# Performance work log

Hardware: AMD Instinct MI355X
Metric: run time of the kernel (lower is better)

## Reference

```python
import jax, jax.numpy as jnp
import numpy as np

B, D = 256, 1024
EPS = 1e-6


def setup_inputs() -> dict:
    key = jax.random.key(0)
    ks = jax.random.split(key, 8)
    s = 1.0 / np.sqrt(D)
    return {
        "x": jax.random.normal(ks[0], (B, D), jnp.float32),
        "Wq": jax.random.normal(ks[1], (D, D), jnp.float32) * s,
        "bq": jax.random.normal(ks[2], (D,), jnp.float32) * 0.01,
        "Wk": jax.random.normal(ks[3], (D, D), jnp.float32) * s,
        "bk": jax.random.normal(ks[4], (D,), jnp.float32) * 0.01,
        "Wv": jax.random.normal(ks[5], (D, D), jnp.float32) * s,
        "bv": jax.random.normal(ks[6], (D,), jnp.float32) * 0.01,
        "scale": jnp.asarray(1.0, jnp.float32),
        "norm_w": jnp.ones((D,), jnp.float32),
    }


def reference(x, Wq, bq, Wk, bk, Wv, bv, scale, norm_w):
    # QKV projections (torch Linear: x @ W.T + b)
    Q = x @ Wq.T + bq  # [B, D]
    K = x @ Wk.T + bk  # [B, D]
    V = x @ Wv.T + bv  # [B, D]
    # outer-product scores [B, D, D]: scores[b,i,j] = Q[b,i]*K[b,j]/scale
    scores = (Q[:, :, None] * K[:, None, :]) / scale
    attn = jax.nn.softmax(scores, axis=-1)  # [B, D, D]
    attended = jnp.einsum("bij,bj->bi", attn, V)  # [B, D]
    # dropout is identity in eval mode
    h = attended + x
    rms = jnp.sqrt(jnp.mean(h * h, axis=-1, keepdims=True) + EPS)
    return (h / rms) * norm_w
```

## Files before the change

### kernel.cpp

```cpp
#include <hip/hip_runtime.h>
#include <hip/hip_bf16.h>

#define BB 256
#define DD 1024

typedef unsigned short u16;
typedef unsigned int   u32;
typedef __attribute__((ext_vector_type(8))) __bf16 bf16x8;
typedef __attribute__((ext_vector_type(4))) float  floatx4;

__device__ __forceinline__ float bf2f(u16 u) {
    union { u32 i; float f; } t; t.i = ((u32)u) << 16; return t.f;
}
__device__ __forceinline__ u16 f2bf_rne(float f) {
    u32 u = __float_as_uint(f);
    u32 r = u + 0x7FFFu + ((u >> 16) & 1u);
    return (u16)(r >> 16);
}
__device__ __forceinline__ bool detect_bf16(const void* p) {
    return (*(const u32*)p) == 0x3F803F80u;
}
__device__ __forceinline__ float loadf(const void* p, int i, bool bf) {
    return bf ? bf2f(((const u16*)p)[i]) : ((const float*)p)[i];
}

__device__ __forceinline__ float wave_sum64(float x) {
    x += __int_as_float(__builtin_amdgcn_update_dpp(0, __float_as_int(x), 0x111, 0xF, 0xF, true));
    x += __int_as_float(__builtin_amdgcn_update_dpp(0, __float_as_int(x), 0x112, 0xF, 0xF, true));
    x += __int_as_float(__builtin_amdgcn_update_dpp(0, __float_as_int(x), 0x114, 0xF, 0xF, true));
    x += __int_as_float(__builtin_amdgcn_update_dpp(0, __float_as_int(x), 0x118, 0xF, 0xF, true));
    x += __int_as_float(__builtin_amdgcn_update_dpp(0, __float_as_int(x), 0x142, 0xA, 0xF, true));
    x += __int_as_float(__builtin_amdgcn_update_dpp(0, __float_as_int(x), 0x143, 0xC, 0xF, true));
    return x;
}

__device__ __forceinline__ void split1(float f, u16& h, u16& l) {
    u32 u  = __float_as_uint(f);
    u32 hu = u & 0xFFFF0000u;
    h = (u16)(hu >> 16);
    l = f2bf_rne(f - __uint_as_float(hu));
}

__global__ __launch_bounds__(256) void qkv_gemm(
    const void* __restrict__ x,
    const void* __restrict__ Wq, const void* __restrict__ bq,
    const void* __restrict__ Wk, const void* __restrict__ bk,
    const void* __restrict__ Wv, const void* __restrict__ bv,
    const void* __restrict__ nw,
    float* __restrict__ qkv)
{
    const bool bf = detect_bf16(nw);
    const int z = blockIdx.z;
    const void* W    = (z == 0) ? Wq : (z == 1) ? Wk : Wv;
    const void* bias = (z == 0) ? bq : (z == 1) ? bk : bv;
    float* outp = qkv + (size_t)z * BB * DD;

    const int m0 = blockIdx.x * 32;
    const int n0 = blockIdx.y * 64;
    const int tid  = threadIdx.x;
    const int lane = tid & 63;
    const int wave = tid >> 6;
    const int wr = wave & 1, wc = wave >> 1;
    const int l15 = lane & 15, quad = lane >> 4;

    __shared__ __align__(16) u16 Ah[32][72], Al[32][72];
    __shared__ __align__(16) u16 Bh[64][72], Bl[64][72];

    const int arow = tid >> 4;
    const int acol = (tid & 15) * 4;

    floatx4 acc[2] = {(floatx4){0.f,0.f,0.f,0.f}, (floatx4){0.f,0.f,0.f,0.f}};

    float4 ar[2], br[4];
    auto ld4 = [&](const void* p, int idx) -> float4 {
        if (!bf) return *(const float4*)((const float*)p + idx);
        const u16* q = (const u16*)p + idx;
        return make_float4(bf2f(q[0]), bf2f(q[1]), bf2f(q[2]), bf2f(q[3]));
    };
    auto fetch = [&](int k0) {
        #pragma unroll
        for (int f = 0; f < 2; ++f) ar[f] = ld4(x, (m0 + arow + f * 16) * DD + k0 + acol);
        #pragma unroll
        for (int f = 0; f < 4; ++f) br[f] = ld4(W, (n0 + arow + f * 16) * DD + k0 + acol);
    };

    fetch(0);
    for (int k0 = 0; k0 < DD; k0 += 64) {
        #pragma unroll
        for (int f = 0; f < 2; ++f) {
            const int r = arow + f * 16;
            ushort4 h, l;
            split1(ar[f].x, h.x, l.x); split1(ar[f].y, h.y, l.y);
            split1(ar[f].z, h.z, l.z); split1(ar[f].w, h.w, l.w);
            *(ushort4*)&Ah[r][acol] = h;
            *(ushort4*)&Al[r][acol] = l;
        }
        #pragma unroll
        for (int f = 0; f < 4; ++f) {
            const int r = arow + f * 16;
            ushort4 h, l;
            split1(br[f].x, h.x, l.x); split1(br[f].y, h.y, l.y);
            split1(br[f].z, h.z, l.z); split1(br[f].w, h.w, l.w);
            *(ushort4*)&Bh[r][acol] = h;
            *(ushort4*)&Bl[r][acol] = l;
        }
        __syncthreads();

        fetch((k0 + 64) & (DD - 1));

        #pragma unroll
        for (int kk = 0; kk < 2; ++kk) {
            const int ko = kk * 32 + quad * 8;
            const bf16x8 ah = *(const bf16x8*)&Ah[wr * 16 + l15][ko];
            const bf16x8 al = *(const bf16x8*)&Al[wr * 16 + l15][ko];
            #pragma unroll
            for (int ni = 0; ni < 2; ++ni) {
                const int brow = wc * 32 + ni * 16 + l15;
                const bf16x8 bh = *(const bf16x8*)&Bh[brow][ko];
                const bf16x8 bl = *(const bf16x8*)&Bl[brow][ko];
                acc[ni] = __builtin_amdgcn_mfma_f32_16x16x32_bf16(al, bh, acc[ni], 0, 0, 0);
                acc[ni] = __builtin_amdgcn_mfma_f32_16x16x32_bf16(ah, bl, acc[ni], 0, 0, 0);
                acc[ni] = __builtin_amdgcn_mfma_f32_16x16x32_bf16(ah, bh, acc[ni], 0, 0, 0);
            }
        }
        __syncthreads();
    }

    #pragma unroll
    for (int ni = 0; ni < 2; ++ni) {
        const int ng = n0 + wc * 32 + ni * 16 + l15;
        const float bv_ = loadf(bias, ng, bf);
        #pragma unroll
        for (int reg = 0; reg < 4; ++reg) {
            const int mg = m0 + wr * 16 + quad * 4 + reg;
            outp[mg * DD + ng] = acc[ni][reg] + bv_;
        }
    }
}

__global__ __launch_bounds__(1024) void attn_norm(
    const float* __restrict__ qkv,
    const void* __restrict__ x,
    const void* __restrict__ scale_p,
    const void* __restrict__ norm_w,
    void* __restrict__ out)
{
    const bool bf = detect_bf16(norm_w);
    const int b = blockIdx.x;
    const int tid = threadIdx.x;
    const int lane = tid & 63;
    const int wave = tid >> 6;

    __shared__ __align__(16) float2 kv[DD];
    __shared__ float wsum[16];

    const float* Qp = qkv + (size_t)b * DD;
    const float* Kp = Qp + (size_t)BB * DD;
    const float* Vp = Qp + 2 * (size_t)BB * DD;
    const float cvt = 1.44269504088896f / loadf(scale_p, 0, bf);

    kv[tid] = make_float2(Kp[tid] * cvt, Vp[tid]);
    __syncthreads();

    const float q   = Qp[tid];
    const float x_l = loadf(x, b * DD + tid, bf);

    float S0 = 0.f, S1 = 0.f, S2 = 0.f, S3 = 0.f;
    float T0 = 0.f, T1 = 0.f, T2 = 0.f, T3 = 0.f;
    const float4* kv4 = (const float4*)kv;
    for (int m = 0; m < DD / 2; m += 4) {
        const float4 p0 = kv4[m + 0];
        const float4 p1 = kv4[m + 1];
        const float4 p2 = kv4[m + 2];
        const float4 p3 = kv4[m + 3];
        float e;
        e = __builtin_amdgcn_exp2f(q * p0.x); S0 += e; T0 = fmaf(e, p0.y, T0);
        e = __builtin_amdgcn_exp2f(q * p0.z); S1 += e; T1 = fmaf(e, p0.w, T1);
        e = __builtin_amdgcn_exp2f(q * p1.x); S2 += e; T2 = fmaf(e, p1.y, T2);
        e = __builtin_amdgcn_exp2f(q * p1.z); S3 += e; T3 = fmaf(e, p1.w, T3);
        e = __builtin_amdgcn_exp2f(q * p2.x); S0 += e; T0 = fmaf(e, p2.y, T0);
        e = __builtin_amdgcn_exp2f(q * p2.z); S1 += e; T1 = fmaf(e, p2.w, T1);
        e = __builtin_amdgcn_exp2f(q * p3.x); S2 += e; T2 = fmaf(e, p3.y, T2);
        e = __builtin_amdgcn_exp2f(q * p3.z); S3 += e; T3 = fmaf(e, p3.w, T3);
    }
    const float S = (S0 + S1) + (S2 + S3);
    const float T = (T0 + T1) + (T2 + T3);
    const float h = fmaf(T, __builtin_amdgcn_rcpf(S), x_l);

    const float ss = wave_sum64(h * h);
    if (lane == 63) wsum[wave] = ss;
    __syncthreads();
    float tot = 0.f;
    #pragma unroll
    for (int w = 0; w < 16; ++w) tot += wsum[w];
    const float rinv = __builtin_amdgcn_rsqf(tot * (1.0f / DD) + 1e-6f);
    const float val = h * rinv * loadf(norm_w, tid, bf);
    const size_t oi = (size_t)b * DD + tid;
    if (bf) ((u16*)out)[oi] = f2bf_rne(val);
    else    ((float*)out)[oi] = val;
}

extern "C" void kernel_launch(void* const* d_in, const int* in_sizes, int n_in,
                              void* d_out, int out_size, void* d_ws, size_t ws_size,
                              hipStream_t stream) {
    const void* x  = d_in[0];
    const void* Wq = d_in[1];
    const void* bq = d_in[2];
    const void* Wk = d_in[3];
    const void* bk = d_in[4];
    const void* Wv = d_in[5];
    const void* bv = d_in[6];
    const void* sc = d_in[7];
    const void* nw = d_in[8];

    float* qkv = (float*)d_ws;

    qkv_gemm<<<dim3(8, 16, 3), 256, 0, stream>>>(x, Wq, bq, Wk, bk, Wv, bv, nw, qkv);
    attn_norm<<<dim3(BB), 1024, 0, stream>>>(qkv, x, sc, nw, d_out);
}
```

Before: 133.6 us.

## Register-tile attention loop over 4 queries × key quarter with packed float2 math

Each thread of the attention kernel now handles 4 query rows over one quarter of the keys instead of one query over all keys. This reuses each LDS key/value load across four queries, cutting LDS traffic per exp, and uses float2 vector types so the compiler can emit packed multiply/FMA instructions. Partial sums are reduced through a new shared buffer with an extra barrier. The cost is more registers and an added reduction step, while the exp count stays the same.

```diff
diff --git a/kernel.cpp b/kernel.cpp
--- a/kernel.cpp
+++ b/kernel.cpp
@@ -8,6 +8,7 @@
 typedef unsigned int   u32;
 typedef __attribute__((ext_vector_type(8))) __bf16 bf16x8;
 typedef __attribute__((ext_vector_type(4))) float  floatx4;
+typedef __attribute__((ext_vector_type(2))) float  floatx2;
 
 __device__ __forceinline__ float bf2f(u16 u) {
     union { u32 i; float f; } t; t.i = ((u32)u) << 16; return t.f;
@@ -150,8 +151,12 @@
     const int tid = threadIdx.x;
     const int lane = tid & 63;
     const int wave = tid >> 6;
-
-    __shared__ __align__(16) float2 kv[DD];
+    const int iq = tid & 255;
+    const int jq = tid >> 8;
+
+    __shared__ __align__(16) float kk[DD];
+    __shared__ __align__(16) float vv[DD];
+    __shared__ float2 part[DD][4];
     __shared__ float wsum[16];
 
     const float* Qp = qkv + (size_t)b * DD;
@@ -159,33 +164,67 @@
     const float* Vp = Qp + 2 * (size_t)BB * DD;
     const float cvt = 1.44269504088896f / loadf(scale_p, 0, bf);
 
-    kv[tid] = make_float2(Kp[tid] * cvt, Vp[tid]);
+    kk[tid] = Kp[tid] * cvt;
+    vv[tid] = Vp[tid];
     __syncthreads();
 
-    const float q   = Qp[tid];
+    const float qv[4] = { Qp[iq], Qp[iq + 256], Qp[iq + 512], Qp[iq + 768] };
+
+    floatx2 S[4][2] = {};
+    floatx2 T[4][2] = {};
+
+    const floatx4* kk4 = (const floatx4*)kk;
+    const floatx4* vv4 = (const floatx4*)vv;
+    const int jb = jq * 64;
+
+    floatx4 kc0 = kk4[jb], kc1 = kk4[jb + 1];
+    floatx4 vc0 = vv4[jb], vc1 = vv4[jb + 1];
+    for (int mo = 0; mo < 64; mo += 2) {
+        const int mn = jb + ((mo + 2) & 63);
+        floatx4 kn0 = kk4[mn], kn1 = kk4[mn + 1];
+        floatx4 vn0 = vv4[mn], vn1 = vv4[mn + 1];
+
+        #pragma unroll
+        for (int g = 0; g < 2; ++g) {
+            const floatx4 K4 = g ? kc1 : kc0;
+            const floatx4 V4 = g ? vc1 : vc0;
+            const floatx2 kA = __builtin_shufflevector(K4, K4, 0, 1);
+            const floatx2 kB = __builtin_shufflevector(K4, K4, 2, 3);
+            const floatx2 vA = __builtin_shufflevector(V4, V4, 0, 1);
+            const floatx2 vB = __builtin_shufflevector(V4, V4, 2, 3);
+            #pragma unroll
+            for (int r = 0; r < 4; ++r) {
+                const float qr = qv[r];
+                const floatx2 aA = kA * qr;
+                const floatx2 aB = kB * qr;
+                floatx2 eA, eB;
+                eA.x = __builtin_amdgcn_exp2f(aA.x);
+                eA.y = __builtin_amdgcn_exp2f(aA.y);
+                eB.x = __builtin_amdgcn_exp2f(aB.x);
+                eB.y = __builtin_amdgcn_exp2f(aB.y);
+                S[r][g] += (eA + eB);
+                T[r][g] = __builtin_elementwise_fma(eA, vA, T[r][g]);
+                T[r][g] = __builtin_elementwise_fma(eB, vB, T[r][g]);
+            }
+        }
+        kc0 = kn0; kc1 = kn1; vc0 = vn0; vc1 = vn1;
+    }
+
+    #pragma unroll
+    for (int r = 0; r < 4; ++r) {
+        const floatx2 Sv = S[r][0] + S[r][1];
+        const floatx2 Tv = T[r][0] + T[r][1];
+        part[iq + r * 256][jq] = make_float2(Sv.x + Sv.y, Tv.x + Tv.y);
+    }
+    __syncthreads();
+
+    const float2 p0 = part[tid][0], p1 = part[tid][1];
+    const float2 p2 = part[tid][2], p3 = part[tid][3];
+    const float Ssum = (p0.x + p1.x) + (p2.x + p3.x);
+    const float Tsum = (p0.y + p1.y) + (p2.y + p3.y);
+
     const float x_l = loadf(x, b * DD + tid, bf);
-
-    float S0 = 0.f, S1 = 0.f, S2 = 0.f, S3 = 0.f;
-    float T0 = 0.f, T1 = 0.f, T2 = 0.f, T3 = 0.f;
-    const float4* kv4 = (const float4*)kv;
-    for (int m = 0; m < DD / 2; m += 4) {
-        const float4 p0 = kv4[m + 0];
-        const float4 p1 = kv4[m + 1];
-        const float4 p2 = kv4[m + 2];
-        const float4 p3 = kv4[m + 3];
-        float e;
-        e = __builtin_amdgcn_exp2f(q * p0.x); S0 += e; T0 = fmaf(e, p0.y, T0);
-        e = __builtin_amdgcn_exp2f(q * p0.z); S1 += e; T1 = fmaf(e, p0.w, T1);
-        e = __builtin_amdgcn_exp2f(q * p1.x); S2 += e; T2 = fmaf(e, p1.y, T2);
-        e = __builtin_amdgcn_exp2f(q * p1.z); S3 += e; T3 = fmaf(e, p1.w, T3);
-        e = __builtin_amdgcn_exp2f(q * p2.x); S0 += e; T0 = fmaf(e, p2.y, T0);
-        e = __builtin_amdgcn_exp2f(q * p2.z); S1 += e; T1 = fmaf(e, p2.w, T1);
-        e = __builtin_amdgcn_exp2f(q * p3.x); S2 += e; T2 = fmaf(e, p3.y, T2);
-        e = __builtin_amdgcn_exp2f(q * p3.z); S3 += e; T3 = fmaf(e, p3.w, T3);
-    }
-    const float S = (S0 + S1) + (S2 + S3);
-    const float T = (T0 + T1) + (T2 + T3);
-    const float h = fmaf(T, __builtin_amdgcn_rcpf(S), x_l);
+    const float h = fmaf(Tsum, __builtin_amdgcn_rcpf(Ssum), x_l);
 
     const float ss = wave_sum64(h * h);
     if (lane == 63) wsum[wave] = ss;
```

Result: faster. 126.5 us (-5.3%).

## Split attention reduction across key halves with register-blocked queries and finalize kernel

Applied to the files above, without the earlier changes.

The attention stage becomes two kernels. The first splits the key dimension into two halves per batch row (twice the blocks), and each thread handles four queries over a 128-key slice so every shared-memory K/V load feeds four exponentials. Partial sums are combined in shared memory and written to workspace. A second kernel merges the two halves and applies the residual add and RMSNorm. The aim is better occupancy and fewer LDS reads per exponential, at the cost of an extra launch and a workspace round trip.

```diff
diff --git a/kernel.cpp b/kernel.cpp
--- a/kernel.cpp
+++ b/kernel.cpp
@@ -138,54 +138,97 @@
     }
 }
 
-__global__ __launch_bounds__(1024) void attn_norm(
+__global__ __launch_bounds__(1024) void attn_part(
     const float* __restrict__ qkv,
+    const void* __restrict__ scale_p,
+    const void* __restrict__ norm_w,
+    float2* __restrict__ pws)
+{
+    const bool bf = detect_bf16(norm_w);
+    const int b   = blockIdx.x;
+    const int jh  = blockIdx.y;
+    const int tid = threadIdx.x;
+    const int iq  = tid & 255;
+    const int jq  = tid >> 8;
+
+    __shared__ __align__(16) float kk[512];
+    __shared__ __align__(16) float vv[512];
+    __shared__ float2 part[DD][4];
+
+    const float* Qp = qkv + (size_t)b * DD;
+    const float* Kp = Qp + (size_t)BB * DD;
+    const float* Vp = Qp + 2 * (size_t)BB * DD;
+    const float cvt = 1.44269504088896f / loadf(scale_p, 0, bf);
+
+    if (tid < 512) {
+        kk[tid] = Kp[jh * 512 + tid] * cvt;
+        vv[tid] = Vp[jh * 512 + tid];
+    }
+    __syncthreads();
+
+    const float q0 = Qp[iq], q1 = Qp[iq + 256], q2 = Qp[iq + 512], q3 = Qp[iq + 768];
+
+    float S0 = 0.f, S1 = 0.f, S2 = 0.f, S3 = 0.f;
+    float T0 = 0.f, T1 = 0.f, T2 = 0.f, T3 = 0.f;
+
+    const floatx4* kk4 = (const floatx4*)kk;
+    const floatx4* vv4 = (const floatx4*)vv;
+    const int jb = jq * 32;
+
+    #pragma unroll 4
+    for (int mo = 0; mo < 32; mo += 2) {
+        const floatx4 Ka = kk4[jb + mo],     Va = vv4[jb + mo];
+        const floatx4 Kb = kk4[jb + mo + 1], Vb = vv4[jb + mo + 1];
+        #pragma unroll
+        for (int g = 0; g < 2; ++g) {
+            const floatx4 K4 = g ? Kb : Ka;
+            const floatx4 V4 = g ? Vb : Va;
+            #pragma unroll
+            for (int c = 0; c < 4; ++c) {
+                const float kc = K4[c], vc = V4[c];
+                float e;
+                e = __builtin_amdgcn_exp2f(kc * q0); S0 += e; T0 = fmaf(e, vc, T0);
+                e = __builtin_amdgcn_exp2f(kc * q1); S1 += e; T1 = fmaf(e, vc, T1);
+                e = __builtin_amdgcn_exp2f(kc * q2); S2 += e; T2 = fmaf(e, vc, T2);
+                e = __builtin_amdgcn_exp2f(kc * q3); S3 += e; T3 = fmaf(e, vc, T3);
+            }
+        }
+    }
+
+    part[iq +   0][jq] = make_float2(S0, T0);
+    part[iq + 256][jq] = make_float2(S1, T1);
+    part[iq + 512][jq] = make_float2(S2, T2);
+    part[iq + 768][jq] = make_float2(S3, T3);
+    __syncthreads();
+
+    const float2 a0 = part[tid][0], a1 = part[tid][1];
+    const float2 a2 = part[tid][2], a3 = part[tid][3];
+    pws[((size_t)b * 2 + jh) * DD + tid] =
+        make_float2((a0.x + a1.x) + (a2.x + a3.x),
+                    (a0.y + a1.y) + (a2.y + a3.y));
+}
+
+__global__ __launch_bounds__(1024) void attn_fin(
+    const float2* __restrict__ pws,
     const void* __restrict__ x,
-    const void* __restrict__ scale_p,
     const void* __restrict__ norm_w,
     void* __restrict__ out)
 {
     const bool bf = detect_bf16(norm_w);
-    const int b = blockIdx.x;
+    const int b   = blockIdx.x;
     const int tid = threadIdx.x;
     const int lane = tid & 63;
     const int wave = tid >> 6;
 
-    __shared__ __align__(16) float2 kv[DD];
     __shared__ float wsum[16];
 
-    const float* Qp = qkv + (size_t)b * DD;
-    const float* Kp = Qp + (size_t)BB * DD;
-    const float* Vp = Qp + 2 * (size_t)BB * DD;
-    const float cvt = 1.44269504088896f / loadf(scale_p, 0, bf);
-
-    kv[tid] = make_float2(Kp[tid] * cvt, Vp[tid]);
-    __syncthreads();
-
-    const float q   = Qp[tid];
+    const float2 p0 = pws[((size_t)b * 2 + 0) * DD + tid];
+    const float2 p1 = pws[((size_t)b * 2 + 1) * DD + tid];
+    const float Ssum = p0.x + p1.x;
+    const float Tsum = p0.y + p1.y;
+
     const float x_l = loadf(x, b * DD + tid, bf);
-
-    float S0 = 0.f, S1 = 0.f, S2 = 0.f, S3 = 0.f;
-    float T0 = 0.f, T1 = 0.f, T2 = 0.f, T3 = 0.f;
-    const float4* kv4 = (const float4*)kv;
-    for (int m = 0; m < DD / 2; m += 4) {
-        const float4 p0 = kv4[m + 0];
-        const float4 p1 = kv4[m + 1];
-        const float4 p2 = kv4[m + 2];
-        const float4 p3 = kv4[m + 3];
-        float e;
-        e = __builtin_amdgcn_exp2f(q * p0.x); S0 += e; T0 = fmaf(e, p0.y, T0);
-        e = __builtin_amdgcn_exp2f(q * p0.z); S1 += e; T1 = fmaf(e, p0.w, T1);
-        e = __builtin_amdgcn_exp2f(q * p1.x); S2 += e; T2 = fmaf(e, p1.y, T2);
-        e = __builtin_amdgcn_exp2f(q * p1.z); S3 += e; T3 = fmaf(e, p1.w, T3);
-        e = __builtin_amdgcn_exp2f(q * p2.x); S0 += e; T0 = fmaf(e, p2.y, T0);
-        e = __builtin_amdgcn_exp2f(q * p2.z); S1 += e; T1 = fmaf(e, p2.w, T1);
-        e = __builtin_amdgcn_exp2f(q * p3.x); S2 += e; T2 = fmaf(e, p3.y, T2);
-        e = __builtin_amdgcn_exp2f(q * p3.z); S3 += e; T3 = fmaf(e, p3.w, T3);
-    }
-    const float S = (S0 + S1) + (S2 + S3);
-    const float T = (T0 + T1) + (T2 + T3);
-    const float h = fmaf(T, __builtin_amdgcn_rcpf(S), x_l);
+    const float h = fmaf(Tsum, __builtin_amdgcn_rcpf(Ssum), x_l);
 
     const float ss = wave_sum64(h * h);
     if (lane == 63) wsum[wave] = ss;
@@ -213,8 +256,10 @@
     const void* sc = d_in[7];
     const void* nw = d_in[8];
 
-    float* qkv = (float*)d_ws;
+    float*  qkv = (float*)d_ws;
+    float2* pws = (float2*)((char*)d_ws + 3u * BB * DD * sizeof(float));
 
     qkv_gemm<<<dim3(8, 16, 3), 256, 0, stream>>>(x, Wq, bq, Wk, bk, Wv, bv, nw, qkv);
-    attn_norm<<<dim3(BB), 1024, 0, stream>>>(qkv, x, sc, nw, d_out);
-}
+    attn_part<<<dim3(BB, 2), 1024, 0, stream>>>(qkv, sc, nw, pws);
+    attn_fin<<<dim3(BB), 1024, 0, stream>>>(pws, x, nw, d_out);
+}
```

Result: no change. 131.2 us (-1.8%).
